# Optimization experiments

Measured on AMD Instinct MI355X. Metric: run time of the kernel, lower is better.

Reference implementation:

```python
import jax, jax.numpy as jnp
import numpy as np
from jax import lax

INPUT_SIZE = 64          # classifier ROI size (init kwarg)
IMG = 640                # source image H=W
PROV, ALPHA, AD = 38, 25, 35
CONF_THRES, IOU_THRES = 0.25, 0.45
MAX_DET = 300            # yolov5 NMS max detections
FLAT = 16 * (INPUT_SIZE // 2) ** 2  # 16384


def setup_inputs() -> dict:
    key = jax.random.key(0)
    ks = jax.random.split(key, 12)
    B, N = 1, 25200
    xy = jax.random.uniform(ks[0], (B, N, 2), minval=32.0, maxval=608.0)
    wh = jax.random.uniform(ks[1], (B, N, 2), minval=16.0, maxval=128.0)
    obj = jax.random.uniform(ks[2], (B, N, 1))
    cls = jax.random.uniform(ks[3], (B, N, 1))
    preds = jnp.concatenate([xy, wh, obj, cls], axis=-1)  # [1,N,6] xywh+obj+cls
    image = jax.random.normal(ks[4], (B, 3, IMG, IMG), dtype=jnp.float32)
    W_conv = 0.1 * jax.random.normal(ks[5], (16, 3, 3, 3), dtype=jnp.float32)
    b_conv = jnp.zeros((16,), jnp.float32)
    W1 = 0.01 * jax.random.normal(ks[6], (8, FLAT, 128), dtype=jnp.float32)
    b1 = jnp.zeros((8, 128), jnp.float32)
    W2p = 0.05 * jax.random.normal(ks[7], (128, PROV), dtype=jnp.float32)
    b2p = jnp.zeros((PROV,), jnp.float32)
    W2a = 0.05 * jax.random.normal(ks[8], (128, ALPHA), dtype=jnp.float32)
    b2a = jnp.zeros((ALPHA,), jnp.float32)
    W2d = 0.05 * jax.random.normal(ks[9], (6, 128, AD), dtype=jnp.float32)
    b2d = jnp.zeros((6, AD), jnp.float32)
    return {"preds": preds, "image": image, "W_conv": W_conv, "b_conv": b_conv,
            "W1": W1, "b1": b1, "W2p": W2p, "b2p": b2p, "W2a": W2a, "b2a": b2a,
            "W2d": W2d, "b2d": b2d}


def _pairwise_iou(b):
    # b: [K,4] xyxy
    x1, y1, x2, y2 = b[:, 0], b[:, 1], b[:, 2], b[:, 3]
    area = (x2 - x1) * (y2 - y1)
    iw = jnp.clip(jnp.minimum(x2[:, None], x2[None, :]) - jnp.maximum(x1[:, None], x1[None, :]), 0.0)
    ih = jnp.clip(jnp.minimum(y2[:, None], y2[None, :]) - jnp.maximum(y1[:, None], y1[None, :]), 0.0)
    inter = iw * ih
    return inter / (area[:, None] + area[None, :] - inter + 1e-7)


def reference(preds, image, W_conv, b_conv, W1, b1, W2p, b2p, W2a, b2a, W2d, b2d):
    # ---- NMS (yolov5-style, single class) ----
    p = preds[0]                                   # [N,6]
    score = p[:, 4] * p[:, 5]                      # obj_conf * cls_conf
    xy, wh = p[:, 0:2], p[:, 2:4]
    boxes = jnp.concatenate([xy - wh / 2, xy + wh / 2], axis=-1)  # xyxy
    masked = jnp.where(score > CONF_THRES, score, -jnp.inf)
    top_s, idx = lax.top_k(masked, MAX_DET)        # sorted desc
    b = boxes[idx]                                 # [K,4]
    valid = top_s > CONF_THRES
    ious = _pairwise_iou(b)                        # [K,K]
    ar = jnp.arange(MAX_DET)

    def body(i, keep):
        sup = jnp.any((ious[i] > IOU_THRES) & keep & (ar < i))
        return keep.at[i].set(keep[i] & jnp.logical_not(sup))

    keep = lax.fori_loop(0, MAX_DET, body, valid)  # greedy suppression

    # ---- fixed-size ROI crop at box top-left (clipped) ----
    x1 = jnp.clip(jnp.round(b[:, 0]).astype(jnp.int32), 0, IMG - INPUT_SIZE)
    y1 = jnp.clip(jnp.round(b[:, 1]).astype(jnp.int32), 0, IMG - INPUT_SIZE)
    img0 = image[0]                                # [3,H,W]
    crops = jax.vmap(lambda y, x: lax.dynamic_slice(img0, (0, y, x), (3, INPUT_SIZE, INPUT_SIZE)))(y1, x1)

    # ---- LicensePlateClassifier: conv->relu->maxpool->flatten->8 heads ----
    conv = lax.conv_general_dilated(crops, W_conv, (1, 1), 'SAME',
                                    dimension_numbers=('NCHW', 'OIHW', 'NCHW'))
    conv = jax.nn.relu(conv + b_conv[None, :, None, None])
    pooled = lax.reduce_window(conv, -jnp.inf, lax.max, (1, 1, 2, 2), (1, 1, 2, 2), 'VALID')
    feats = pooled.reshape(MAX_DET, FLAT)          # NCHW flatten == torch.flatten(x,1)
    h = jax.nn.relu(jnp.einsum('kf,hfd->hkd', feats, W1) + b1[:, None, :])  # [8,K,128]
    out_p = h[0] @ W2p + b2p                       # [K,38]
    out_a = h[1] @ W2a + b2a                       # [K,25]
    out_d = jnp.einsum('hkd,hdo->hko', h[2:], W2d) + b2d[:, None, :]        # [6,K,35]
    out_d = out_d.transpose(1, 0, 2).reshape(MAX_DET, 6 * AD)
    logits = jnp.concatenate([out_p, out_a, out_d], axis=1)  # [K,273]
    return logits * keep.astype(logits.dtype)[:, None]
```

## Files before the change

kernel.cpp:

```cpp
#include <hip/hip_runtime.h>

#define N_PRED 25200
#define CONF 0.25f
#define IOU_THR 0.45f
#define MAXD 300
#define IMGW 640
#define CROPW 64
#define HISTN 16640

typedef float f32x4 __attribute__((ext_vector_type(4)));
typedef short s16x8 __attribute__((ext_vector_type(8)));
typedef unsigned long long u64;

#define OFF_HIST   0u
#define OFF_CNT    66560u
#define OFF_CUT    66624u
#define OFF_CAND   66816u
#define CTRL_BYTES 75008u
#define OFF_BOXES  75008u
#define OFF_XY1    79872u
#define OFF_VALID  82432u
#define OFF_KEEP   83712u
#define OFF_SUP    84992u
#define OFF_H      97024u
#define OFF_FEATS  1325824u
#define OFF_PART   11811584u

__device__ inline unsigned short f2bf(float x) {
  unsigned u = __float_as_uint(x);
  u += 0x7FFFu + ((u >> 16) & 1u);
  return (unsigned short)(u >> 16);
}

__global__ __launch_bounds__(256) void k_hist(const float* __restrict__ preds,
                                              unsigned* __restrict__ hist) {
  int i = blockIdx.x * 256 + threadIdx.x;
  if (i >= N_PRED) return;
  float s = preds[i * 6 + 4] * preds[i * 6 + 5];
  if (s > CONF) atomicAdd(&hist[__float_as_uint(s) >> 16], 1u);
}

__global__ __launch_bounds__(256) void k_findcut(const unsigned* __restrict__ hist,
                                                 unsigned* __restrict__ cut) {
  __shared__ unsigned s[256];
  int t = threadIdx.x;
  int base = t * 65;
  unsigned local = 0;
  for (int i = 0; i < 65; ++i) local += hist[base + i];
  s[t] = local;
  __syncthreads();
  for (int off = 1; off < 256; off <<= 1) {
    unsigned add = (t + off < 256) ? s[t + off] : 0u;
    __syncthreads();
    s[t] += add;
    __syncthreads();
  }
  unsigned incl = s[t];
  unsigned excl = (t < 255) ? s[t + 1] : 0u;
  if (incl >= (unsigned)MAXD && excl < (unsigned)MAXD) {
    unsigned acc = excl, res = 0u;
    #pragma unroll
    for (int ii = 64; ii >= 0; --ii) {
      acc += hist[base + ii];
      if (res == 0u && acc >= (unsigned)MAXD) res = (unsigned)(base + ii);
    }
    cut[0] = res;
  }
}

__global__ __launch_bounds__(256) void k_compact(const float* __restrict__ preds,
                                                 const unsigned* __restrict__ cut,
                                                 unsigned* __restrict__ cnt,
                                                 u64* __restrict__ cand) {
  int i = blockIdx.x * 256 + threadIdx.x;
  if (i >= N_PRED) return;
  float s = preds[i * 6 + 4] * preds[i * 6 + 5];
  if (s <= CONF) return;
  unsigned bits = __float_as_uint(s);
  if ((bits >> 16) < cut[0]) return;
  unsigned pos = atomicAdd(cnt, 1u);
  if (pos < 1024u)
    cand[pos] = ((u64)bits << 32) | (u64)(0xFFFFFFFFu - (unsigned)i);
}

__global__ __launch_bounds__(1024) void k_sortprep(const float* __restrict__ preds,
                                                   const u64* __restrict__ cand,
                                                   float* __restrict__ boxes,
                                                   int* __restrict__ xy1,
                                                   float* __restrict__ validf) {
  __shared__ u64 sk[1024];
  int t = threadIdx.x;
  sk[t] = cand[t];
  __syncthreads();
  for (int k = 2; k <= 1024; k <<= 1)
    for (int j = k >> 1; j > 0; j >>= 1) {
      int p = t ^ j;
      if (p > t) {
        u64 a = sk[t], b = sk[p];
        bool up = ((t & k) == 0);
        bool sw = up ? (a < b) : (a > b);
        if (sw) { sk[t] = b; sk[p] = a; }
      }
      __syncthreads();
    }
  if (t < MAXD) {
    u64 key = sk[t];
    if (key != 0ull) {
      int idx = (int)(0xFFFFFFFFu - (unsigned)(key & 0xFFFFFFFFull));
      float cx = preds[idx * 6 + 0], cy = preds[idx * 6 + 1];
      float w  = preds[idx * 6 + 2], h  = preds[idx * 6 + 3];
      float x1 = cx - w * 0.5f, y1 = cy - h * 0.5f;
      float x2 = cx + w * 0.5f, y2 = cy + h * 0.5f;
      boxes[t * 4 + 0] = x1; boxes[t * 4 + 1] = y1;
      boxes[t * 4 + 2] = x2; boxes[t * 4 + 3] = y2;
      int xi = (int)rintf(x1); xi = min(max(xi, 0), IMGW - CROPW);
      int yi = (int)rintf(y1); yi = min(max(yi, 0), IMGW - CROPW);
      xy1[t * 2 + 0] = xi; xy1[t * 2 + 1] = yi;
      validf[t] = 1.0f;
    } else {
      boxes[t * 4 + 0] = 0.f; boxes[t * 4 + 1] = 0.f;
      boxes[t * 4 + 2] = 0.f; boxes[t * 4 + 3] = 0.f;
      xy1[t * 2 + 0] = 0; xy1[t * 2 + 1] = 0;
      validf[t] = 0.f;
    }
  }
}

__global__ __launch_bounds__(320) void k_iou(const float* __restrict__ boxes,
                                             u64* __restrict__ sup) {
  int i = blockIdx.x, t = threadIdx.x;
  int w = t >> 6, lane = t & 63;
  f32x4 bi = *(const f32x4*)&boxes[i * 4];
  f32x4 bj = (t < MAXD) ? *(const f32x4*)&boxes[t * 4]
                        : (f32x4){0.f, 0.f, 0.f, 0.f};
  float ar  = (bi[2] - bi[0]) * (bi[3] - bi[1]);
  float arj = (bj[2] - bj[0]) * (bj[3] - bj[1]);
  float iw = fmaxf(fminf(bi[2], bj[2]) - fmaxf(bi[0], bj[0]), 0.f);
  float ih = fmaxf(fminf(bi[3], bj[3]) - fmaxf(bi[1], bj[1]), 0.f);
  float inter = iw * ih;
  float iou = inter / (ar + arj - inter + 1e-7f);
  u64 bm = __ballot((t < MAXD) && (iou > IOU_THR));
  if (lane == 0) sup[i * 5 + w] = bm;
}

__global__ __launch_bounds__(64) void k_nms(const u64* __restrict__ sup,
                                            const float* __restrict__ validf,
                                            float* __restrict__ keepf) {
  int lane = threadIdx.x;
  u64 srow[5][5];
  #pragma unroll
  for (int c = 0; c < 5; ++c)
    #pragma unroll
    for (int ww = 0; ww < 5; ++ww) srow[c][ww] = 0ull;
  #pragma unroll
  for (int c = 0; c < 5; ++c) {
    int i = c * 64 + lane;
    if (i < MAXD) {
      #pragma unroll
      for (int ww = 0; ww <= c; ++ww) srow[c][ww] = sup[i * 5 + ww];
    }
  }
  u64 validm[5];
  #pragma unroll
  for (int c = 0; c < 5; ++c) {
    int i = c * 64 + lane;
    float vf = (i < MAXD) ? validf[i] : 0.f;
    validm[c] = __ballot(vf > 0.5f);
  }
  u64 kw0 = 0, kw1 = 0, kw2 = 0, kw3 = 0;
  #pragma unroll
  for (int c = 0; c < 5; ++c) {
    bool ext = ((srow[c][0] & kw0) | (srow[c][1] & kw1) |
                (srow[c][2] & kw2) | (srow[c][3] & kw3)) != 0ull;
    u64 alive = validm[c] & __ballot(!ext);
    unsigned mlo = (unsigned)srow[c][c], mhi = (unsigned)(srow[c][c] >> 32);
    u64 rem = alive;
    while (rem) {
      int b = (int)__builtin_ctzll(rem);
      u64 gt = (b == 63) ? 0ull : (~0ull << (b + 1));
      u64 mi = ((u64)(unsigned)__builtin_amdgcn_readlane((int)mhi, b) << 32) |
               (u64)(unsigned)__builtin_amdgcn_readlane((int)mlo, b);
      alive &= ~(mi & gt);
      rem = alive & gt;
    }
    int i = c * 64 + lane;
    if (i < MAXD) keepf[i] = ((alive >> lane) & 1ull) ? 1.f : 0.f;
    if (c == 0) kw0 = alive;
    else if (c == 1) kw1 = alive;
    else if (c == 2) kw2 = alive;
    else if (c == 3) kw3 = alive;
  }
}

__global__ __launch_bounds__(256) void k_cropconv(const float* __restrict__ image,
                                                  const float* __restrict__ Wc,
                                                  const float* __restrict__ bc,
                                                  const int* __restrict__ xy1,
                                                  short* __restrict__ feats) {
  __shared__ __align__(16) float crop[3][10][68];
  int det = blockIdx.x, sl = blockIdx.y, tid = threadIdx.x;
  int pr0 = sl * 4;
  int gyBase = pr0 * 2 - 1;
  int ch = tid >> 4, px = tid & 15;

  float w[27];
  #pragma unroll
  for (int i = 0; i < 27; i++) w[i] = Wc[ch * 27 + i];
  float bias = bc[ch];

  int x0 = xy1[det * 2 + 0], y0 = xy1[det * 2 + 1];
  float sv[8];
  #pragma unroll
  for (int i = 0; i < 8; i++) {
    int u = tid + i * 256;
    float v = 0.f;
    if (u < 1920) {
      int row = u >> 6, x = u & 63;
      int c = row / 10, ry = row - c * 10;
      int gy = gyBase + ry;
      if (gy >= 0 && gy < CROPW)
        v = image[(size_t)c * (IMGW * IMGW) + (y0 + gy) * IMGW + x0 + x];
    }
    sv[i] = v;
  }
  if (tid < 120) {
    int row = tid >> 2, e = tid & 3;
    int c = row / 10, ry = row - c * 10;
    crop[c][ry][(e == 0) ? 0 : (64 + e)] = 0.f;
  }
  #pragma unroll
  for (int i = 0; i < 8; i++) {
    int u = tid + i * 256;
    if (u < 1920) {
      int row = u >> 6, x = u & 63;
      int c = row / 10, ry = row - c * 10;
      crop[c][ry][x + 1] = sv[i];
    }
  }
  __syncthreads();
  #pragma unroll
  for (int pr = 0; pr < 4; pr++) {
    float acc0[4] = {0.f, 0.f, 0.f, 0.f};
    float acc1[4] = {0.f, 0.f, 0.f, 0.f};
    #pragma unroll
    for (int c = 0; c < 3; c++) {
      #pragma unroll
      for (int r = 0; r < 4; r++) {
        const float* rp = &crop[c][2 * pr + r][4 * px];
        f32x4 v4 = *(const f32x4*)rp;
        float2 v2 = *(const float2*)(rp + 4);
        float in[6] = {v4[0], v4[1], v4[2], v4[3], v2.x, v2.y};
        if (r <= 2) {
          const float w0 = w[c * 9 + r * 3], w1 = w[c * 9 + r * 3 + 1],
                      w2 = w[c * 9 + r * 3 + 2];
          #pragma unroll
          for (int q = 0; q < 4; q++)
            acc0[q] += in[q] * w0 + in[q + 1] * w1 + in[q + 2] * w2;
        }
        if (r >= 1) {
          const float w0 = w[c * 9 + (r - 1) * 3], w1 = w[c * 9 + (r - 1) * 3 + 1],
                      w2 = w[c * 9 + (r - 1) * 3 + 2];
          #pragma unroll
          for (int q = 0; q < 4; q++)
            acc1[q] += in[q] * w0 + in[q + 1] * w1 + in[q + 2] * w2;
        }
      }
    }
    float m0 = fmaxf(fmaxf(acc0[0], acc0[1]), fmaxf(acc1[0], acc1[1]));
    float m1 = fmaxf(fmaxf(acc0[2], acc0[3]), fmaxf(acc1[2], acc1[3]));
    unsigned lo = f2bf(fmaxf(m0 + bias, 0.f));
    unsigned hi = f2bf(fmaxf(m1 + bias, 0.f));
    *(unsigned*)&feats[(size_t)det * 16384 + ch * 1024 + (pr0 + pr) * 32 + 2 * px] =
        lo | (hi << 16);
  }
}

__global__ __launch_bounds__(512, 2) void k_gemm(const short* __restrict__ feats,
                                                 const float* __restrict__ W1,
                                                 float* __restrict__ part,
                                                 int ntiles) {
  __shared__ __align__(16) short As[2][320 * 64];
  int tid = threadIdx.x;
  int wid = tid >> 6, lane = tid & 63;
  int wm = wid & 3, wn = wid >> 2;
  int lr = lane & 15, kg = lane >> 4;
  int ks = blockIdx.x, hd = blockIdx.y, dh = blockIdx.z;
  const int f0 = ks * ntiles * 64, d0 = dh * 64;
  const float* w1h = W1 + (size_t)hd * 16384 * 128;

  f32x4 acc[5][2];
  #pragma unroll
  for (int i = 0; i < 5; i++)
    #pragma unroll
    for (int j = 0; j < 2; j++) acc[i][j] = (f32x4){0.f, 0.f, 0.f, 0.f};

  s16x8 aR[5];
  #pragma unroll
  for (int i = 0; i < 5; i++) {
    int ch = tid + i * 512, m = ch >> 3, c = ch & 7;
    aR[i] = *(const s16x8*)(feats + (size_t)m * 16384 + f0 + c * 8);
  }
  const float* bp = w1h + (size_t)(f0 + kg * 8) * 128 + d0 + wn * 32 + lr;
  float bF[2][2][8];
  #pragma unroll
  for (int k32 = 0; k32 < 2; k32++)
    #pragma unroll
    for (int nf = 0; nf < 2; nf++)
      #pragma unroll
      for (int j = 0; j < 8; j++)
        bF[k32][nf][j] = bp[(k32 * 32 + j) * 128 + nf * 16];
  #pragma unroll
  for (int i = 0; i < 5; i++) {
    int ch = tid + i * 512, m = ch >> 3, c = ch & 7;
    *(s16x8*)((char*)&As[0][0] + m * 128 + ((c ^ (m & 7)) << 4)) = aR[i];
  }
  __syncthreads();

  for (int t = 0; t < ntiles; ++t) {
    int cur = t & 1;
    s16x8 bfr[2][2];
    #pragma unroll
    for (int k32 = 0; k32 < 2; k32++)
      #pragma unroll
      for (int nf = 0; nf < 2; nf++)
        #pragma unroll
        for (int j = 0; j < 8; j++)
          bfr[k32][nf][j] = (short)f2bf(bF[k32][nf][j]);
    bool pf = (t + 1) < ntiles;
    if (pf) {
      int f1 = f0 + (t + 1) * 64;
      #pragma unroll
      for (int i = 0; i < 5; i++) {
        int ch = tid + i * 512, m = ch >> 3, c = ch & 7;
        aR[i] = *(const s16x8*)(feats + (size_t)m * 16384 + f1 + c * 8);
      }
      const float* bp2 = bp + (size_t)(t + 1) * 64 * 128;
      #pragma unroll
      for (int k32 = 0; k32 < 2; k32++)
        #pragma unroll
        for (int nf = 0; nf < 2; nf++)
          #pragma unroll
          for (int j = 0; j < 8; j++)
            bF[k32][nf][j] = bp2[(k32 * 32 + j) * 128 + nf * 16];
    }
    #pragma unroll
    for (int k32 = 0; k32 < 2; ++k32) {
      s16x8 af[5];
      #pragma unroll
      for (int mf = 0; mf < 5; ++mf) {
        int row = wm * 80 + mf * 16 + lr;
        int c = k32 * 4 + kg;
        af[mf] = *(const s16x8*)((const char*)&As[cur][0] + row * 128 + ((c ^ (row & 7)) << 4));
      }
      #pragma unroll
      for (int nf = 0; nf < 2; ++nf)
        #pragma unroll
        for (int mf = 0; mf < 5; ++mf)
          acc[mf][nf] = __builtin_amdgcn_mfma_f32_16x16x32_bf16(af[mf], bfr[k32][nf], acc[mf][nf], 0, 0, 0);
    }
    if (pf) {
      #pragma unroll
      for (int i = 0; i < 5; i++) {
        int ch = tid + i * 512, m = ch >> 3, c = ch & 7;
        *(s16x8*)((char*)&As[cur ^ 1][0] + m * 128 + ((c ^ (m & 7)) << 4)) = aR[i];
      }
      __syncthreads();
    }
  }
  #pragma unroll
  for (int mf = 0; mf < 5; ++mf)
    #pragma unroll
    for (int nf = 0; nf < 2; ++nf)
      #pragma unroll
      for (int r = 0; r < 4; ++r) {
        int m = wm * 80 + mf * 16 + kg * 4 + r;
        int d = d0 + wn * 32 + nf * 16 + lr;
        part[(((size_t)ks * 8 + hd) * 320 + m) * 128 + d] = acc[mf][nf][r];
      }
}

__global__ __launch_bounds__(256) void k_reduce(const float* __restrict__ part,
                                                const float* __restrict__ b1,
                                                float* __restrict__ h,
                                                int nks) {
  int o = blockIdx.x * 256 + threadIdx.x;
  int d = o & 127;
  int k = (o >> 7) % 300;
  int hh = o / (128 * 300);
  float s = 0.f;
  for (int ksp = 0; ksp < nks; ksp++)
    s += part[(((size_t)ksp * 8 + hh) * 320 + k) * 128 + d];
  s += b1[hh * 128 + d];
  h[o] = fmaxf(s, 0.f);
}

__global__ __launch_bounds__(320) void k_fc2(const float* __restrict__ h,
                                             const float* __restrict__ keepf,
                                             const float* __restrict__ W2p,
                                             const float* __restrict__ b2p,
                                             const float* __restrict__ W2a,
                                             const float* __restrict__ b2a,
                                             const float* __restrict__ W2d,
                                             const float* __restrict__ b2d,
                                             float* __restrict__ out) {
  int det = blockIdx.x, t = threadIdx.x;
  __shared__ float hl[1024];
  for (int i = t; i < 1024; i += 320) {
    int hh = i >> 7, d = i & 127;
    hl[i] = h[((size_t)hh * 300 + det) * 128 + d];
  }
  __syncthreads();
  if (t >= 273) return;
  float kf = keepf[det];
  float s = 0.f, bias;
  if (t < 38) {
    const float* hp = hl;
    for (int d = 0; d < 128; d++) s += hp[d] * W2p[d * 38 + t];
    bias = b2p[t];
  } else if (t < 63) {
    int c = t - 38;
    const float* hp = hl + 128;
    for (int d = 0; d < 128; d++) s += hp[d] * W2a[d * 25 + c];
    bias = b2a[c];
  } else {
    int u = t - 63, j = u / 35, o = u - j * 35;
    const float* hp = hl + (2 + j) * 128;
    for (int d = 0; d < 128; d++) s += hp[d] * W2d[((size_t)j * 128 + d) * 35 + o];
    bias = b2d[j * 35 + o];
  }
  out[det * 273 + t] = (s + bias) * kf;
}

extern "C" void kernel_launch(void* const* d_in, const int* in_sizes, int n_in,
                              void* d_out, int out_size, void* d_ws, size_t ws_size,
                              hipStream_t stream) {
  (void)in_sizes; (void)n_in; (void)out_size;
  const float* preds = (const float*)d_in[0];
  const float* image = (const float*)d_in[1];
  const float* Wc    = (const float*)d_in[2];
  const float* bc    = (const float*)d_in[3];
  const float* W1    = (const float*)d_in[4];
  const float* b1    = (const float*)d_in[5];
  const float* W2p   = (const float*)d_in[6];
  const float* b2p   = (const float*)d_in[7];
  const float* W2a   = (const float*)d_in[8];
  const float* b2a   = (const float*)d_in[9];
  const float* W2d   = (const float*)d_in[10];
  const float* b2d   = (const float*)d_in[11];

  char* ws = (char*)d_ws;
  unsigned* hist   = (unsigned*)(ws + OFF_HIST);
  unsigned* cnt    = (unsigned*)(ws + OFF_CNT);
  unsigned* cut    = (unsigned*)(ws + OFF_CUT);
  u64*      cand   = (u64*)(ws + OFF_CAND);
  float*    boxes  = (float*)(ws + OFF_BOXES);
  int*      xy1    = (int*)(ws + OFF_XY1);
  float*    validf = (float*)(ws + OFF_VALID);
  float*    keepf  = (float*)(ws + OFF_KEEP);
  u64*      sup    = (u64*)(ws + OFF_SUP);
  float*    hbuf   = (float*)(ws + OFF_H);
  short*    feats  = (short*)(ws + OFF_FEATS);
  float*    part   = (float*)(ws + OFF_PART);
  float*    out    = (float*)d_out;

  int nks = (ws_size >= (size_t)OFF_PART + 32ull * 8 * 320 * 128 * 4) ? 32 : 16;
  int ntiles = 256 / nks;

  hipMemsetAsync(ws, 0, CTRL_BYTES, stream);
  k_hist<<<(N_PRED + 255) / 256, 256, 0, stream>>>(preds, hist);
  k_findcut<<<1, 256, 0, stream>>>(hist, cut);
  k_compact<<<(N_PRED + 255) / 256, 256, 0, stream>>>(preds, cut, cnt, cand);
  k_sortprep<<<1, 1024, 0, stream>>>(preds, cand, boxes, xy1, validf);
  k_iou<<<MAXD, 320, 0, stream>>>(boxes, sup);
  k_nms<<<1, 64, 0, stream>>>(sup, validf, keepf);
  k_cropconv<<<dim3(300, 8), 256, 0, stream>>>(image, Wc, bc, xy1, feats);
  k_gemm<<<dim3(nks, 8, 2), 512, 0, stream>>>(feats, W1, part, ntiles);
  k_reduce<<<1200, 256, 0, stream>>>(part, b1, hbuf, nks);
  k_fc2<<<MAXD, 320, 0, stream>>>(hbuf, keepf, W2p, b2p, W2a, b2a, W2d, b2d, out);
}
```

Before: 138.8 us.

## Load GEMM A tiles directly into LDS via global_load_lds, single-buffered

Replaces the register-staged A-tile load in k_gemm with direct global-to-LDS loads (global_load_lds, 16 bytes) that carry the XOR swizzle in the global address. It drops the LDS double buffer to a single buffer and raises the launch bound from 2 to 4 blocks per CU, so more blocks can be resident and fewer registers are spent on staging. The cost is that A loads are no longer overlapped with the MFMA work: each tile is loaded after a barrier and waited on before compute, which exposes load latency.

```diff
diff --git a/kernel.cpp b/kernel.cpp
--- a/kernel.cpp
+++ b/kernel.cpp
@@ -30,6 +30,12 @@
   unsigned u = __float_as_uint(x);
   u += 0x7FFFu + ((u >> 16) & 1u);
   return (unsigned short)(u >> 16);
+}
+
+__device__ inline void gload_lds16(const void* g, void* l) {
+  __builtin_amdgcn_global_load_lds(
+      (const __attribute__((address_space(1))) void*)g,
+      (__attribute__((address_space(3))) void*)l, 16, 0, 0);
 }
 
 __global__ __launch_bounds__(256) void k_hist(const float* __restrict__ preds,
@@ -275,11 +281,11 @@
   }
 }
 
-__global__ __launch_bounds__(512, 2) void k_gemm(const short* __restrict__ feats,
+__global__ __launch_bounds__(512, 4) void k_gemm(const short* __restrict__ feats,
                                                  const float* __restrict__ W1,
                                                  float* __restrict__ part,
                                                  int ntiles) {
-  __shared__ __align__(16) short As[2][320 * 64];
+  __shared__ __align__(16) short As[320 * 64];
   int tid = threadIdx.x;
   int wid = tid >> 6, lane = tid & 63;
   int wm = wid & 3, wn = wid >> 2;
@@ -288,17 +294,21 @@
   const int f0 = ks * ntiles * 64, d0 = dh * 64;
   const float* w1h = W1 + (size_t)hd * 16384 * 128;
 
+  int gm = (wid * 5) * 8 + (lane >> 3);
+  int gc = lane & 7;
+  char* ldsbase = (char*)As + wid * 5120;
+
   f32x4 acc[5][2];
   #pragma unroll
   for (int i = 0; i < 5; i++)
     #pragma unroll
     for (int j = 0; j < 2; j++) acc[i][j] = (f32x4){0.f, 0.f, 0.f, 0.f};
 
-  s16x8 aR[5];
   #pragma unroll
   for (int i = 0; i < 5; i++) {
-    int ch = tid + i * 512, m = ch >> 3, c = ch & 7;
-    aR[i] = *(const s16x8*)(feats + (size_t)m * 16384 + f0 + c * 8);
+    int m = gm + i * 8;
+    gload_lds16(feats + (size_t)m * 16384 + f0 + ((gc ^ (m & 7)) << 3),
+                ldsbase + i * 1024);
   }
   const float* bp = w1h + (size_t)(f0 + kg * 8) * 128 + d0 + wn * 32 + lr;
   float bF[2][2][8];
@@ -309,15 +319,9 @@
       #pragma unroll
       for (int j = 0; j < 8; j++)
         bF[k32][nf][j] = bp[(k32 * 32 + j) * 128 + nf * 16];
-  #pragma unroll
-  for (int i = 0; i < 5; i++) {
-    int ch = tid + i * 512, m = ch >> 3, c = ch & 7;
-    *(s16x8*)((char*)&As[0][0] + m * 128 + ((c ^ (m & 7)) << 4)) = aR[i];
-  }
   __syncthreads();
 
   for (int t = 0; t < ntiles; ++t) {
-    int cur = t & 1;
     s16x8 bfr[2][2];
     #pragma unroll
     for (int k32 = 0; k32 < 2; k32++)
@@ -328,12 +332,6 @@
           bfr[k32][nf][j] = (short)f2bf(bF[k32][nf][j]);
     bool pf = (t + 1) < ntiles;
     if (pf) {
-      int f1 = f0 + (t + 1) * 64;
-      #pragma unroll
-      for (int i = 0; i < 5; i++) {
-        int ch = tid + i * 512, m = ch >> 3, c = ch & 7;
-        aR[i] = *(const s16x8*)(feats + (size_t)m * 16384 + f1 + c * 8);
-      }
       const float* bp2 = bp + (size_t)(t + 1) * 64 * 128;
       #pragma unroll
       for (int k32 = 0; k32 < 2; k32++)
@@ -350,7 +348,7 @@
       for (int mf = 0; mf < 5; ++mf) {
         int row = wm * 80 + mf * 16 + lr;
         int c = k32 * 4 + kg;
-        af[mf] = *(const s16x8*)((const char*)&As[cur][0] + row * 128 + ((c ^ (row & 7)) << 4));
+        af[mf] = *(const s16x8*)((const char*)As + row * 128 + ((c ^ (row & 7)) << 4));
       }
       #pragma unroll
       for (int nf = 0; nf < 2; ++nf)
@@ -359,10 +357,13 @@
           acc[mf][nf] = __builtin_amdgcn_mfma_f32_16x16x32_bf16(af[mf], bfr[k32][nf], acc[mf][nf], 0, 0, 0);
     }
     if (pf) {
+      __syncthreads();
+      int f1 = f0 + (t + 1) * 64;
       #pragma unroll
       for (int i = 0; i < 5; i++) {
-        int ch = tid + i * 512, m = ch >> 3, c = ch & 7;
-        *(s16x8*)((char*)&As[cur ^ 1][0] + m * 128 + ((c ^ (m & 7)) << 4)) = aR[i];
+        int m = gm + i * 8;
+        gload_lds16(feats + (size_t)m * 16384 + f1 + ((gc ^ (m & 7)) << 3),
+                    ldsbase + i * 1024);
       }
       __syncthreads();
     }
```

Result: slower. 155.5 us (+12.0%).
